# Performance work log

Measured on AMD Instinct MI355X. Metric: run time of the kernel, lower is better.

Reference implementation:

```python
import jax, jax.numpy as jnp
import numpy as np

DIM = 1024
N_EXPERTS = 8
TOP_K = 2
B, S = 2, 1024


def setup_inputs() -> dict:
    key = jax.random.key(0)
    ks = jax.random.split(key, 4)
    scale = 0.02
    return {
        "u_t": jax.random.normal(ks[0], (B, S, DIM), dtype=jnp.float32),
        "centroids": jax.random.normal(ks[1], (N_EXPERTS, DIM), dtype=jnp.float32),
        "score_biases": jnp.zeros((N_EXPERTS,), dtype=jnp.float32),
        "W1": jax.random.normal(ks[2], (N_EXPERTS, DIM, 4 * DIM), dtype=jnp.float32) * scale,
        "b1": jnp.zeros((N_EXPERTS, 4 * DIM), dtype=jnp.float32),
        "W2": jax.random.normal(ks[3], (N_EXPERTS, 4 * DIM, DIM), dtype=jnp.float32) * scale,
        "b2": jnp.zeros((N_EXPERTS, DIM), dtype=jnp.float32),
    }


def reference(u_t, centroids, score_biases, W1, b1, W2, b2):
    Bs, Ss, dim = u_t.shape
    T = Bs * Ss
    N = centroids.shape[0]
    K = TOP_K

    u_flat = u_t.reshape(T, dim)
    scores = u_flat @ centroids.T + score_biases          # [T, N]
    gate = jax.nn.softmax(scores, axis=-1)                # [T, N]
    topk_vals, topk_idx = jax.lax.top_k(gate, K)          # [T, K]

    flat_idx = topk_idx.reshape(-1)                       # [T*K]

    # load-violation stats (no grad path; pure counts)
    perfect_load = K * T / N
    f_i = jnp.zeros((N,), dtype=jnp.float32).at[flat_idx].add(1.0)
    maxvio = (jnp.max(f_i) - perfect_load) / perfect_load

    # Grouped MLP expressed as dense per-expert compute over all tokens,
    # then combined with a sparse [T, N] gate matrix (same math as masked dispatch).
    h = jax.nn.relu(jnp.einsum("td,ndh->nth", u_flat, W1) + b1[:, None, :])  # [N, T, 4*dim]
    expert_outs = jnp.einsum("nth,nhd->ntd", h, W2) + b2[:, None, :]          # [N, T, dim]

    rows = jnp.repeat(jnp.arange(T), K)
    combine_w = jnp.zeros((T, N), dtype=topk_vals.dtype).at[rows, flat_idx].add(topk_vals.reshape(-1))
    out = jnp.einsum("tn,ntd->td", combine_w, expert_outs).reshape(Bs, Ss, dim)
    return (out, maxvio)
```

## Files before the change

### kernel.cpp

```cpp
#include <hip/hip_runtime.h>
#include <hip/hip_bf16.h>

#define T_TOK 2048
#define DIMS  1024
#define HID   4096
#define NE    8

typedef __bf16 bf16x8 __attribute__((ext_vector_type(8)));
typedef float  f32x4  __attribute__((ext_vector_type(4)));

__device__ __forceinline__ unsigned short f2bf(float f) {
  unsigned u = __float_as_uint(f);
  u += 0x7FFFu + ((u >> 16) & 1u);
  return (unsigned short)(u >> 16);
}

__device__ __forceinline__ void g2l16(const void* g, void* l) {
  __builtin_amdgcn_global_load_lds((const __attribute__((address_space(1))) void*)g,
                                   (__attribute__((address_space(3))) void*)l,
                                   16, 0, 0);
}

__global__ __launch_bounds__(256) void k_zero(int* cnt) {
  if (threadIdx.x < NE) cnt[threadIdx.x] = 0;
}

__global__ __launch_bounds__(256) void k_route(const float* __restrict__ u,
    const float* __restrict__ cent, const float* __restrict__ sbias,
    int* __restrict__ topk_idx, float* __restrict__ topk_val, int* __restrict__ cnt) {
  int wave = threadIdx.x >> 6;
  int lane = threadIdx.x & 63;
  int t = blockIdx.x * 4 + wave;
  const float* ur = u + (size_t)t * DIMS;
  float p[NE];
#pragma unroll
  for (int n = 0; n < NE; n++) p[n] = 0.f;
#pragma unroll
  for (int ch = 0; ch < 4; ch++) {
    int d = ch * 256 + lane * 4;
    float4 uv = *(const float4*)(ur + d);
#pragma unroll
    for (int n = 0; n < NE; n++) {
      float4 cv = *(const float4*)(cent + n * DIMS + d);
      p[n] += uv.x * cv.x + uv.y * cv.y + uv.z * cv.z + uv.w * cv.w;
    }
  }
#pragma unroll
  for (int n = 0; n < NE; n++) {
#pragma unroll
    for (int o = 32; o > 0; o >>= 1) p[n] += __shfl_xor(p[n], o);
  }
  if (lane == 0) {
    float g[NE];
    float m = -1e30f;
#pragma unroll
    for (int n = 0; n < NE; n++) { g[n] = p[n] + sbias[n]; m = fmaxf(m, g[n]); }
    float sum = 0.f;
#pragma unroll
    for (int n = 0; n < NE; n++) { g[n] = expf(g[n] - m); sum += g[n]; }
    float inv = 1.f / sum;
#pragma unroll
    for (int n = 0; n < NE; n++) g[n] *= inv;
    int i0 = 0;
#pragma unroll
    for (int n = 1; n < NE; n++) if (g[n] > g[i0]) i0 = n;
    int i1 = (i0 == 0) ? 1 : 0;
#pragma unroll
    for (int n = 0; n < NE; n++) if (n != i0 && g[n] > g[i1]) i1 = n;
    topk_idx[2 * t] = i0;     topk_idx[2 * t + 1] = i1;
    topk_val[2 * t] = g[i0];  topk_val[2 * t + 1] = g[i1];
    atomicAdd(&cnt[i0], 1);
    atomicAdd(&cnt[i1], 1);
  }
}

__global__ __launch_bounds__(64) void k_finalize(const int* __restrict__ cnt,
    int* __restrict__ offs, int* __restrict__ cursor, float* __restrict__ maxvio) {
  if (threadIdx.x == 0) {
    int o = 0, mx = 0;
#pragma unroll
    for (int n = 0; n < NE; n++) { offs[n] = o; o += cnt[n]; mx = max(mx, cnt[n]); }
    maxvio[0] = ((float)mx - 512.f) / 512.f;
#pragma unroll
    for (int n = 0; n < NE; n++) cursor[n] = 0;
  }
}

__global__ __launch_bounds__(256) void k_place(const int* __restrict__ topk_idx,
    const int* __restrict__ offs, int* __restrict__ cursor,
    int* __restrict__ rowtok, int* __restrict__ pairpos) {
  int t = blockIdx.x * 256 + threadIdx.x;
  if (t >= T_TOK) return;
#pragma unroll
  for (int k = 0; k < 2; k++) {
    int e = topk_idx[2 * t + k];
    int pos = atomicAdd(&cursor[e], 1);
    rowtok[offs[e] + pos] = t;
    pairpos[2 * t + k] = offs[e] + pos;
  }
}

__global__ __launch_bounds__(256) void k_cvt_u(const float* __restrict__ u,
                                               unsigned short* __restrict__ ub) {
  int i = (blockIdx.x * 256 + threadIdx.x) * 8;
  float4 a = *(const float4*)(u + i);
  float4 b = *(const float4*)(u + i + 4);
  union { unsigned short us[8]; uint4 v; } r;
  r.us[0] = f2bf(a.x); r.us[1] = f2bf(a.y); r.us[2] = f2bf(a.z); r.us[3] = f2bf(a.w);
  r.us[4] = f2bf(b.x); r.us[5] = f2bf(b.y); r.us[6] = f2bf(b.z); r.us[7] = f2bf(b.w);
  *(uint4*)(ub + i) = r.v;
}

__global__ __launch_bounds__(256) void k_cvt_w(const float* __restrict__ W,
    unsigned short* __restrict__ out, int R, int C) {
  __shared__ float tile[64][65];
  int e = blockIdx.z;
  size_t base = (size_t)e * R * C;
  int r0 = blockIdx.y * 64, c0 = blockIdx.x * 64;
  int tr  = threadIdx.x >> 4;
  int tc4 = (threadIdx.x & 15) * 4;
#pragma unroll
  for (int it = 0; it < 4; it++) {
    int row = tr + it * 16;
    float4 v = *(const float4*)(W + base + (size_t)(r0 + row) * C + c0 + tc4);
    tile[row][tc4] = v.x; tile[row][tc4 + 1] = v.y; tile[row][tc4 + 2] = v.z; tile[row][tc4 + 3] = v.w;
  }
  __syncthreads();
  int c = threadIdx.x >> 2;
  int seg = (threadIdx.x & 3) * 16;
  union { unsigned short us[8]; uint4 v; } r;
#pragma unroll
  for (int half = 0; half < 2; half++) {
#pragma unroll
    for (int i = 0; i < 8; i++) r.us[i] = f2bf(tile[seg + half * 8 + i][c]);
    *(uint4*)(out + base + (size_t)(c0 + c) * R + r0 + seg + half * 8) = r.v;
  }
}

#define BM 128
#define BN 128
#define BK 64

__global__ __launch_bounds__(256) void k_gemm1(const unsigned short* __restrict__ ub,
    const unsigned short* __restrict__ w1t, const float* __restrict__ b1,
    const int* __restrict__ rowtok, const int* __restrict__ cnts, const int* __restrict__ offs,
    unsigned short* __restrict__ h) {
  int e = blockIdx.z;
  int cnt = cnts[e];
  int m0 = blockIdx.y * BM;
  if (m0 >= cnt) return;
  int off = offs[e];
  int n0 = blockIdx.x * BN;
  __shared__ __align__(16) unsigned char smem[32768];

  int tid = threadIdx.x;
  int lane = tid & 63;
  int wm = (tid >> 7) & 1;
  int wn = (tid >> 6) & 1;
  int srow = tid >> 3;
  int cp = tid & 7;
  const unsigned short* gA[4];
  const unsigned short* gB[4];
#pragma unroll
  for (int a = 0; a < 4; a++) {
    int r = a * 32 + srow;
    int c = cp ^ (r & 7);
    int pr = min(off + m0 + r, off + cnt - 1);
    int tok = rowtok[pr];
    gA[a] = ub + (size_t)tok * DIMS + c * 8;
    gB[a] = w1t + ((size_t)e * HID + (n0 + r)) * DIMS + c * 8;
  }
  int wboff = __builtin_amdgcn_readfirstlane((tid >> 6) << 10);
  f32x4 acc[4][4];
  f32x4 zz = {0.f, 0.f, 0.f, 0.f};
#pragma unroll
  for (int i = 0; i < 4; i++)
#pragma unroll
    for (int j = 0; j < 4; j++) acc[i][j] = zz;

  int lane15 = lane & 15, quad = lane >> 4, l7 = lane & 7;
  unsigned aRowOff = (unsigned)((wm * 64 + lane15) * 128);
  unsigned bRowOff = (unsigned)(16384 + (wn * 64 + lane15) * 128);

#pragma unroll 1
  for (int k0 = 0; k0 < DIMS; k0 += BK) {
#pragma unroll
    for (int a = 0; a < 4; a++) g2l16(gA[a] + k0, smem + a * 4096 + wboff);
#pragma unroll
    for (int a = 0; a < 4; a++) g2l16(gB[a] + k0, smem + 16384 + a * 4096 + wboff);
    __syncthreads();
#pragma unroll
    for (int s = 0; s < 2; s++) {
      unsigned cpf = (unsigned)(((s * 4 + quad) ^ l7) * 16);
      bf16x8 af[4], bfr[4];
#pragma unroll
      for (int i = 0; i < 4; i++) af[i] = *(const bf16x8*)(smem + aRowOff + i * 2048 + cpf);
#pragma unroll
      for (int j = 0; j < 4; j++) bfr[j] = *(const bf16x8*)(smem + bRowOff + j * 2048 + cpf);
#pragma unroll
      for (int i = 0; i < 4; i++)
#pragma unroll
        for (int j = 0; j < 4; j++)
          acc[i][j] = __builtin_amdgcn_mfma_f32_16x16x32_bf16(af[i], bfr[j], acc[i][j], 0, 0, 0);
    }
    __syncthreads();
  }
  float b1v[4];
#pragma unroll
  for (int j = 0; j < 4; j++) b1v[j] = b1[e * HID + n0 + wn * 64 + j * 16 + lane15];
#pragma unroll
  for (int i = 0; i < 4; i++) {
#pragma unroll
    for (int r = 0; r < 4; r++) {
      int mrow = m0 + wm * 64 + i * 16 + quad * 4 + r;
      if (mrow < cnt) {
        size_t hrow = (size_t)(off + mrow) * HID;
#pragma unroll
        for (int j = 0; j < 4; j++) {
          int col = n0 + wn * 64 + j * 16 + lane15;
          float v = fmaxf(acc[i][j][r] + b1v[j], 0.f);
          h[hrow + col] = f2bf(v);
        }
      }
    }
  }
}

__global__ __launch_bounds__(256) void k_gemm2(const unsigned short* __restrict__ hbuf,
    const unsigned short* __restrict__ w2t, const float* __restrict__ b2,
    const int* __restrict__ cnts, const int* __restrict__ offs,
    float* __restrict__ pout) {
  int e = blockIdx.z;
  int cnt = cnts[e];
  int m0 = blockIdx.y * BM;
  if (m0 >= cnt) return;
  int off = offs[e];
  int n0 = blockIdx.x * BN;
  __shared__ __align__(16) unsigned char smem[32768];

  int tid = threadIdx.x;
  int lane = tid & 63;
  int wm = (tid >> 7) & 1;
  int wn = (tid >> 6) & 1;
  int srow = tid >> 3;
  int cp = tid & 7;
  const unsigned short* gA[4];
  const unsigned short* gB[4];
#pragma unroll
  for (int a = 0; a < 4; a++) {
    int r = a * 32 + srow;
    int c = cp ^ (r & 7);
    int pr = min(off + m0 + r, off + cnt - 1);
    gA[a] = hbuf + (size_t)pr * HID + c * 8;
    gB[a] = w2t + ((size_t)e * DIMS + (n0 + r)) * HID + c * 8;
  }
  int wboff = __builtin_amdgcn_readfirstlane((tid >> 6) << 10);
  f32x4 acc[4][4];
  f32x4 zz = {0.f, 0.f, 0.f, 0.f};
#pragma unroll
  for (int i = 0; i < 4; i++)
#pragma unroll
    for (int j = 0; j < 4; j++) acc[i][j] = zz;

  int lane15 = lane & 15, quad = lane >> 4, l7 = lane & 7;
  unsigned aRowOff = (unsigned)((wm * 64 + lane15) * 128);
  unsigned bRowOff = (unsigned)(16384 + (wn * 64 + lane15) * 128);

#pragma unroll 1
  for (int k0 = 0; k0 < HID; k0 += BK) {
#pragma unroll
    for (int a = 0; a < 4; a++) g2l16(gA[a] + k0, smem + a * 4096 + wboff);
#pragma unroll
    for (int a = 0; a < 4; a++) g2l16(gB[a] + k0, smem + 16384 + a * 4096 + wboff);
    __syncthreads();
#pragma unroll
    for (int s = 0; s < 2; s++) {
      unsigned cpf = (unsigned)(((s * 4 + quad) ^ l7) * 16);
      bf16x8 af[4], bfr[4];
#pragma unroll
      for (int i = 0; i < 4; i++) af[i] = *(const bf16x8*)(smem + aRowOff + i * 2048 + cpf);
#pragma unroll
      for (int j = 0; j < 4; j++) bfr[j] = *(const bf16x8*)(smem + bRowOff + j * 2048 + cpf);
#pragma unroll
      for (int i = 0; i < 4; i++)
#pragma unroll
        for (int j = 0; j < 4; j++)
          acc[i][j] = __builtin_amdgcn_mfma_f32_16x16x32_bf16(af[i], bfr[j], acc[i][j], 0, 0, 0);
    }
    __syncthreads();
  }
  float b2v[4];
#pragma unroll
  for (int j = 0; j < 4; j++) b2v[j] = b2[e * DIMS + n0 + wn * 64 + j * 16 + lane15];
#pragma unroll
  for (int i = 0; i < 4; i++) {
#pragma unroll
    for (int r = 0; r < 4; r++) {
      int mrow = m0 + wm * 64 + i * 16 + quad * 4 + r;
      if (mrow < cnt) {
        size_t prow = (size_t)(off + mrow) * DIMS;
#pragma unroll
        for (int j = 0; j < 4; j++) {
          int col = n0 + wn * 64 + j * 16 + lane15;
          pout[prow + col] = acc[i][j][r] + b2v[j];
        }
      }
    }
  }
}

__global__ __launch_bounds__(256) void k_combine(const float* __restrict__ pout,
    const int* __restrict__ pairpos, const float* __restrict__ tkv,
    float* __restrict__ out) {
  int t = blockIdx.x;
  int d = threadIdx.x * 4;
  int p0 = pairpos[2 * t], p1 = pairpos[2 * t + 1];
  float w0 = tkv[2 * t], w1 = tkv[2 * t + 1];
  float4 a = *(const float4*)(pout + (size_t)p0 * DIMS + d);
  float4 b = *(const float4*)(pout + (size_t)p1 * DIMS + d);
  float4 o;
  o.x = w0 * a.x + w1 * b.x;
  o.y = w0 * a.y + w1 * b.y;
  o.z = w0 * a.z + w1 * b.z;
  o.w = w0 * a.w + w1 * b.w;
  *(float4*)(out + (size_t)t * DIMS + d) = o;
}

extern "C" void kernel_launch(void* const* d_in, const int* in_sizes, int n_in,
                              void* d_out, int out_size, void* d_ws, size_t ws_size,
                              hipStream_t stream) {
  const float* u     = (const float*)d_in[0];
  const float* cent  = (const float*)d_in[1];
  const float* sbias = (const float*)d_in[2];
  const float* W1    = (const float*)d_in[3];
  const float* b1    = (const float*)d_in[4];
  const float* W2    = (const float*)d_in[5];
  const float* b2    = (const float*)d_in[6];
  float* out = (float*)d_out;

  char* ws = (char*)d_ws;
  unsigned short* wT   = (unsigned short*)(ws);
  unsigned short* ubuf = (unsigned short*)(ws + 67108864);
  unsigned short* hbuf = (unsigned short*)(ws + 71303168);
  float*          pout = (float*)(ws + 104857600);
  char* r = ws + 121634816;
  int*   cnt      = (int*)(r);
  int*   offs     = (int*)(r + 64);
  int*   cursor   = (int*)(r + 128);
  int*   topk_idx = (int*)(r + 256);
  float* topk_val = (float*)(r + 256 + 16384);
  int*   rowtok   = (int*)(r + 256 + 32768);
  int*   pairpos  = (int*)(r + 256 + 49152);

  k_zero<<<1, 256, 0, stream>>>(cnt);
  k_route<<<512, 256, 0, stream>>>(u, cent, sbias, topk_idx, topk_val, cnt);
  k_finalize<<<1, 64, 0, stream>>>(cnt, offs, cursor, out + 2097152);
  k_place<<<8, 256, 0, stream>>>(topk_idx, offs, cursor, rowtok, pairpos);
  k_cvt_u<<<1024, 256, 0, stream>>>(u, ubuf);
  k_cvt_w<<<dim3(64, 16, 8), 256, 0, stream>>>(W1, wT, 1024, 4096);
  k_gemm1<<<dim3(32, 16, 8), 256, 0, stream>>>(ubuf, wT, b1, rowtok, cnt, offs, hbuf);
  k_cvt_w<<<dim3(16, 64, 8), 256, 0, stream>>>(W2, wT, 4096, 1024);
  k_gemm2<<<dim3(8, 16, 8), 256, 0, stream>>>(hbuf, wT, b2, cnt, offs, pout);
  k_combine<<<2048, 256, 0, stream>>>(pout, pairpos, topk_val, out);
}
```

Before: 521.3 us.

## Split-K the second expert GEMM and reduce the partial sums in combine

```diff
diff --git a/kernel.cpp b/kernel.cpp
--- a/kernel.cpp
+++ b/kernel.cpp
@@ -229,8 +229,10 @@
 __global__ __launch_bounds__(256) void k_gemm2(const unsigned short* __restrict__ hbuf,
     const unsigned short* __restrict__ w2t, const float* __restrict__ b2,
     const int* __restrict__ cnts, const int* __restrict__ offs,
-    float* __restrict__ pout) {
-  int e = blockIdx.z;
+    float* __restrict__ pout, int KC) {
+  int z = blockIdx.z;
+  int e = z & 7;
+  int sp = z >> 3;
   int cnt = cnts[e];
   int m0 = blockIdx.y * BM;
   if (m0 >= cnt) return;
@@ -266,8 +268,9 @@
   unsigned aRowOff = (unsigned)((wm * 64 + lane15) * 128);
   unsigned bRowOff = (unsigned)(16384 + (wn * 64 + lane15) * 128);
 
+  int kbeg = sp * KC, kend = kbeg + KC;
 #pragma unroll 1
-  for (int k0 = 0; k0 < HID; k0 += BK) {
+  for (int k0 = kbeg; k0 < kend; k0 += BK) {
 #pragma unroll
     for (int a = 0; a < 4; a++) g2l16(gA[a] + k0, smem + a * 4096 + wboff);
 #pragma unroll
@@ -291,7 +294,9 @@
   }
   float b2v[4];
 #pragma unroll
-  for (int j = 0; j < 4; j++) b2v[j] = b2[e * DIMS + n0 + wn * 64 + j * 16 + lane15];
+  for (int j = 0; j < 4; j++)
+    b2v[j] = (sp == 0) ? b2[e * DIMS + n0 + wn * 64 + j * 16 + lane15] : 0.f;
+  float* pme = pout + (size_t)sp * T_TOK * 2 * DIMS;
 #pragma unroll
   for (int i = 0; i < 4; i++) {
 #pragma unroll
@@ -302,7 +307,7 @@
 #pragma unroll
         for (int j = 0; j < 4; j++) {
           int col = n0 + wn * 64 + j * 16 + lane15;
-          pout[prow + col] = acc[i][j][r] + b2v[j];
+          pme[prow + col] = acc[i][j][r] + b2v[j];
         }
       }
     }
@@ -311,13 +316,19 @@
 
 __global__ __launch_bounds__(256) void k_combine(const float* __restrict__ pout,
     const int* __restrict__ pairpos, const float* __restrict__ tkv,
-    float* __restrict__ out) {
+    float* __restrict__ out, int nsplit) {
   int t = blockIdx.x;
   int d = threadIdx.x * 4;
   int p0 = pairpos[2 * t], p1 = pairpos[2 * t + 1];
   float w0 = tkv[2 * t], w1 = tkv[2 * t + 1];
-  float4 a = *(const float4*)(pout + (size_t)p0 * DIMS + d);
-  float4 b = *(const float4*)(pout + (size_t)p1 * DIMS + d);
+  float4 a = {0.f, 0.f, 0.f, 0.f}, b = {0.f, 0.f, 0.f, 0.f};
+  const size_t SSTRIDE = (size_t)T_TOK * 2 * DIMS;
+  for (int s = 0; s < nsplit; s++) {
+    float4 av = *(const float4*)(pout + s * SSTRIDE + (size_t)p0 * DIMS + d);
+    float4 bv = *(const float4*)(pout + s * SSTRIDE + (size_t)p1 * DIMS + d);
+    a.x += av.x; a.y += av.y; a.z += av.z; a.w += av.w;
+    b.x += bv.x; b.y += bv.y; b.z += bv.z; b.w += bv.w;
+  }
   float4 o;
   o.x = w0 * a.x + w1 * b.x;
   o.y = w0 * a.y + w1 * b.y;
@@ -342,8 +353,11 @@
   unsigned short* wT   = (unsigned short*)(ws);
   unsigned short* ubuf = (unsigned short*)(ws + 67108864);
   unsigned short* hbuf = (unsigned short*)(ws + 71303168);
-  float*          pout = (float*)(ws + 104857600);
-  char* r = ws + 121634816;
+  const size_t POUT_OFF = 104857600ull;
+  const size_t PSZ = (size_t)T_TOK * 2 * DIMS * 4;
+  int nsplit = (ws_size >= POUT_OFF + 4 * PSZ + (1u << 20)) ? 4 : 1;
+  float* pout4 = (float*)(ws + POUT_OFF);
+  char* r = ws + POUT_OFF + (size_t)nsplit * PSZ;
   int*   cnt      = (int*)(r);
   int*   offs     = (int*)(r + 64);
   int*   cursor   = (int*)(r + 128);
@@ -360,6 +374,7 @@
   k_cvt_w<<<dim3(64, 16, 8), 256, 0, stream>>>(W1, wT, 1024, 4096);
   k_gemm1<<<dim3(32, 16, 8), 256, 0, stream>>>(ubuf, wT, b1, rowtok, cnt, offs, hbuf);
   k_cvt_w<<<dim3(16, 64, 8), 256, 0, stream>>>(W2, wT, 4096, 1024);
-  k_gemm2<<<dim3(8, 16, 8), 256, 0, stream>>>(hbuf, wT, b2, cnt, offs, pout);
-  k_combine<<<2048, 256, 0, stream>>>(pout, pairpos, topk_val, out);
-}
+  k_gemm2<<<dim3(8, 16, 8 * nsplit), 256, 0, stream>>>(hbuf, wT, b2, cnt, offs,
+                                                       pout4, HID / nsplit);
+  k_combine<<<2048, 256, 0, stream>>>(pout4, pairpos, topk_val, out, nsplit);
+}
```

Measured after the change: 504.9 us. 1.03x faster.
